# Performance work log

Hardware: AMD Instinct MI355X
Metric: run time of the kernel (lower is better)

The kernel has to match this reference:

```python
import jax, jax.numpy as jnp
import numpy as np

U, I, D, E, L = 100000, 50000, 64, 600000, 3
N = U + I  # total nodes in bipartite graph


def setup_inputs() -> dict:
    key = jax.random.key(0)
    k1, k2, k3, k4 = jax.random.split(key, 4)
    user_emb = jax.random.normal(k1, (U, D), dtype=jnp.float32) * 0.1
    item_emb = jax.random.normal(k2, (I, D), dtype=jnp.float32) * 0.1
    # random user-item interactions; symmetrize to build the (U+I)x(U+I) adjacency
    u = jax.random.randint(k3, (E,), 0, U)
    i = jax.random.randint(k4, (E,), 0, I) + U
    edge_src = jnp.concatenate([u, i])  # [2E]
    edge_dst = jnp.concatenate([i, u])  # [2E]
    # symmetric normalization: A_hat[s,d] = 1/sqrt(deg_s * deg_d)
    deg = jax.ops.segment_sum(jnp.ones((2 * E,), jnp.float32), edge_dst, num_segments=N)
    dinv = jnp.where(deg > 0, 1.0 / jnp.sqrt(deg), 0.0)
    edge_vals = dinv[edge_src] * dinv[edge_dst]
    return {
        "user_emb": user_emb,
        "item_emb": item_emb,
        "edge_src": edge_src,
        "edge_dst": edge_dst,
        "edge_vals": edge_vals,
    }


def reference(user_emb, item_emb, edge_src, edge_dst, edge_vals):
    # LightGCN propagation: ego_{k+1} = A_hat @ ego_k, then mean over the L layer outputs
    ego = jnp.concatenate([user_emb, item_emb], axis=0)  # [N, D]
    acc = jnp.zeros_like(ego)
    for _ in range(L):  # fixed small layer count
        msgs = edge_vals[:, None] * ego[edge_src]  # [2E, D] gather + scale
        ego = jax.ops.segment_sum(msgs, edge_dst, num_segments=N)  # SpMM via scatter-add
        acc = acc + ego
    mean_emb = acc / L
    return mean_emb[:U], mean_emb[U:]
```

## Files before the change

### kernel.cpp

```cpp
#include <hip/hip_runtime.h>

#define U_CNT 100000
#define I_CNT 50000
#define D_DIM 64
#define N_NODES 150000
#define CHUNK 2048
#define NBKT 586
#define SCAN_BLK 512
#define CCAP 3584

__device__ __forceinline__ float blo(unsigned u) { return __uint_as_float(u << 16); }
__device__ __forceinline__ float bhi(unsigned u) { return __uint_as_float(u & 0xFFFF0000u); }
__device__ __forceinline__ unsigned f2b(float f) {
    unsigned b = __float_as_uint(f);
    return (b + 0x7FFFu + ((b >> 16) & 1u)) >> 16;
}
__device__ __forceinline__ unsigned pack2(float a, float b) {
    return f2b(a) | (f2b(b) << 16);
}

__global__ void bucket_hist(const int* __restrict__ dst, int* __restrict__ H,
                            int NB_B, int nE,
                            const float4* __restrict__ user4,
                            const float4* __restrict__ item4,
                            uint2* __restrict__ ego0, int n4u, int n4) {
    __shared__ int h[NBKT];
    for (int i = threadIdx.x; i < NBKT; i += blockDim.x) h[i] = 0;
    __syncthreads();
    int b = blockIdx.x;
    int beg = b * CHUNK, end = min(nE, beg + CHUNK);
    for (int e = beg + (int)threadIdx.x; e < end; e += blockDim.x)
        atomicAdd(&h[dst[e] >> 8], 1);
    __syncthreads();
    for (int i = threadIdx.x; i < NBKT; i += blockDim.x) H[i * NB_B + b] = h[i];
    int gsz = gridDim.x * blockDim.x;
    for (int i = blockIdx.x * blockDim.x + threadIdx.x; i < n4; i += gsz) {
        float4 f = (i < n4u) ? user4[i] : item4[i - n4u];
        ego0[i] = make_uint2(pack2(f.x, f.y), pack2(f.z, f.w));
    }
}

__global__ void block_sums(const int* __restrict__ in, int* __restrict__ blksum, int n) {
    __shared__ int sm[SCAN_BLK];
    int i = blockIdx.x * SCAN_BLK + threadIdx.x;
    sm[threadIdx.x] = (i < n) ? in[i] : 0;
    __syncthreads();
    for (int off = SCAN_BLK / 2; off > 0; off >>= 1) {
        if (threadIdx.x < off) sm[threadIdx.x] += sm[threadIdx.x + off];
        __syncthreads();
    }
    if (threadIdx.x == 0) blksum[blockIdx.x] = sm[0];
}

__global__ void scan_blksums(const int* __restrict__ blksum, int* __restrict__ blkoff, int nb) {
    __shared__ int sm[1024];
    int t = threadIdx.x;
    int v = (t < nb) ? blksum[t] : 0;
    sm[t] = v;
    __syncthreads();
    for (int off = 1; off < 1024; off <<= 1) {
        int x = (t >= off) ? sm[t - off] : 0;
        __syncthreads();
        sm[t] += x;
        __syncthreads();
    }
    if (t < nb) blkoff[t] = sm[t] - v;
}

__global__ void scan_within(int* __restrict__ H, const int* __restrict__ blkoff, int n) {
    __shared__ int sm[SCAN_BLK];
    int i = blockIdx.x * SCAN_BLK + threadIdx.x;
    int t = threadIdx.x;
    int d = (i < n) ? H[i] : 0;
    sm[t] = d;
    __syncthreads();
    for (int off = 1; off < SCAN_BLK; off <<= 1) {
        int x = (t >= off) ? sm[t - off] : 0;
        __syncthreads();
        sm[t] += x;
        __syncthreads();
    }
    if (i < n) H[i] = blkoff[blockIdx.x] + sm[t] - d;
}

__global__ void bucket_scatter(const int* __restrict__ src, const int* __restrict__ dst,
                               const float* __restrict__ val, const int* __restrict__ Hs,
                               uint2* __restrict__ tmp, int NB_B, int nE) {
    __shared__ int cur[NBKT];
    int b = blockIdx.x;
    for (int i = threadIdx.x; i < NBKT; i += blockDim.x) cur[i] = Hs[i * NB_B + b];
    __syncthreads();
    int beg = b * CHUNK, end = min(nE, beg + CHUNK);
    for (int e = beg + (int)threadIdx.x; e < end; e += blockDim.x) {
        int d = dst[e];
        int pos = atomicAdd(&cur[d >> 8], 1);
        tmp[pos] = make_uint2((unsigned)src[e] | ((unsigned)(d & 255) << 18),
                              __float_as_uint(val[e]));
    }
}

__global__ void bucket_build(const int* __restrict__ Hs, const uint2* __restrict__ tmp,
                             int2* __restrict__ csr, int* __restrict__ row_ptr,
                             int NB_B, int nE) {
    __shared__ int hist[256];
    __shared__ int scanbuf[256];
    __shared__ int cur[256];
    __shared__ uint2 cache[CCAP];
    int bkt  = blockIdx.x;
    int base = Hs[(size_t)bkt * NB_B];
    int endp = (bkt + 1 < NBKT) ? Hs[(size_t)(bkt + 1) * NB_B] : nE;
    int size = endp - base;
    int nbins = min(256, N_NODES - bkt * 256);
    int t = threadIdx.x;

    hist[t] = 0;
    __syncthreads();
    bool cached = (size <= CCAP);
    for (int k = t; k < size; k += blockDim.x) {
        uint2 r = tmp[base + k];
        if (cached) cache[k] = r;
        atomicAdd(&hist[(r.x >> 18) & 255], 1);
    }
    __syncthreads();
    int v = hist[t];
    scanbuf[t] = v;
    __syncthreads();
    for (int off = 1; off < 256; off <<= 1) {
        int x = (t >= off) ? scanbuf[t - off] : 0;
        __syncthreads();
        scanbuf[t] += x;
        __syncthreads();
    }
    int ex = scanbuf[t] - v;
    if (t < nbins) row_ptr[bkt * 256 + t] = base + ex;
    cur[t] = ex;
    __syncthreads();
    if (bkt == NBKT - 1) {
        if (t == 0) row_ptr[N_NODES] = nE;
        if (t < 4)  csr[nE + t] = make_int2(0, 0);
    }
    for (int k = t; k < size; k += blockDim.x) {
        uint2 r = cached ? cache[k] : tmp[base + k];
        int f = (r.x >> 18) & 255;
        int p = atomicAdd(&cur[f], 1);
        csr[base + p] = make_int2((int)(r.x & 0x3FFFFu), (int)r.y);
    }
}

__global__ void deg_scatter(const int* __restrict__ row_ptr, int* __restrict__ perm) {
    __shared__ int h[256];
    __shared__ int scanbuf[256];
    int t = threadIdx.x;
    int base = blockIdx.x * 256;
    int n = base + t;
    bool valid = (n < N_NODES);
    int deg = valid ? (row_ptr[n + 1] - row_ptr[n]) : 0;
    int bin = 255 - min(deg, 255);
    h[t] = 0;
    __syncthreads();
    int rank = 0;
    if (valid) rank = atomicAdd(&h[bin], 1);
    __syncthreads();
    int v = h[t];
    scanbuf[t] = v;
    __syncthreads();
    for (int off = 1; off < 256; off <<= 1) {
        int x = (t >= off) ? scanbuf[t - off] : 0;
        __syncthreads();
        scanbuf[t] += x;
        __syncthreads();
    }
    __syncthreads();
    if (valid) {
        int ex = scanbuf[bin] - h[bin];
        perm[base + ex + rank] = n;
    }
}

__device__ __forceinline__ void fma8(float (&acc)[8], float v, uint4 g) {
    acc[0] = fmaf(v, blo(g.x), acc[0]); acc[1] = fmaf(v, bhi(g.x), acc[1]);
    acc[2] = fmaf(v, blo(g.y), acc[2]); acc[3] = fmaf(v, bhi(g.y), acc[3]);
    acc[4] = fmaf(v, blo(g.z), acc[4]); acc[5] = fmaf(v, bhi(g.z), acc[5]);
    acc[6] = fmaf(v, blo(g.w), acc[6]); acc[7] = fmaf(v, bhi(g.w), acc[7]);
}

template <int FINAL>
__global__ void lgcn_spmm(const int* __restrict__ row_ptr,
                          const int2* __restrict__ csr,
                          const uint4* __restrict__ ego_in,
                          uint4* __restrict__ ego_out,
                          const uint4* __restrict__ egoA,
                          const uint4* __restrict__ egoB,
                          float4* __restrict__ out,
                          const int* __restrict__ perm) {
    int widx = (blockIdx.x * blockDim.x + threadIdx.x) >> 3;
    int l    = threadIdx.x & 7;
    if (widx >= N_NODES) return;
    int node = perm[widx];
    int beg = row_ptr[node];
    int end = row_ptr[node + 1];

    float a0[8] = {0, 0, 0, 0, 0, 0, 0, 0};
    float a1[8] = {0, 0, 0, 0, 0, 0, 0, 0};

    int2 e0 = csr[beg], e1 = csr[beg + 1], e2 = csr[beg + 2], e3 = csr[beg + 3];
    int j = beg;
    while (j + 4 <= end) {
        uint4 x0 = ego_in[(size_t)e0.x * 8 + l];
        uint4 x1 = ego_in[(size_t)e1.x * 8 + l];
        uint4 x2 = ego_in[(size_t)e2.x * 8 + l];
        uint4 x3 = ego_in[(size_t)e3.x * 8 + l];
        int2 n0 = csr[j + 4], n1 = csr[j + 5], n2 = csr[j + 6], n3 = csr[j + 7];
        fma8(a0, __int_as_float(e0.y), x0);
        fma8(a1, __int_as_float(e1.y), x1);
        fma8(a0, __int_as_float(e2.y), x2);
        fma8(a1, __int_as_float(e3.y), x3);
        e0 = n0; e1 = n1; e2 = n2; e3 = n3;
        j += 4;
    }
    int rem = end - j;
    if (rem > 0) fma8(a0, __int_as_float(e0.y), ego_in[(size_t)e0.x * 8 + l]);
    if (rem > 1) fma8(a1, __int_as_float(e1.y), ego_in[(size_t)e1.x * 8 + l]);
    if (rem > 2) fma8(a0, __int_as_float(e2.y), ego_in[(size_t)e2.x * 8 + l]);

    float acc[8];
#pragma unroll
    for (int k = 0; k < 8; ++k) acc[k] = a0[k] + a1[k];

    if (!FINAL) {
        uint4 r;
        r.x = pack2(acc[0], acc[1]); r.y = pack2(acc[2], acc[3]);
        r.z = pack2(acc[4], acc[5]); r.w = pack2(acc[6], acc[7]);
        ego_out[(size_t)node * 8 + l] = r;
    } else {
        uint4 a = egoA[(size_t)node * 8 + l];
        uint4 b = egoB[(size_t)node * 8 + l];
        const float s = 1.0f / 3.0f;
        float4 o0, o1;
        o0.x = (blo(a.x) + blo(b.x) + acc[0]) * s;
        o0.y = (bhi(a.x) + bhi(b.x) + acc[1]) * s;
        o0.z = (blo(a.y) + blo(b.y) + acc[2]) * s;
        o0.w = (bhi(a.y) + bhi(b.y) + acc[3]) * s;
        o1.x = (blo(a.z) + blo(b.z) + acc[4]) * s;
        o1.y = (bhi(a.z) + bhi(b.z) + acc[5]) * s;
        o1.z = (blo(a.w) + blo(b.w) + acc[6]) * s;
        o1.w = (bhi(a.w) + bhi(b.w) + acc[7]) * s;
        size_t ob = (size_t)node * 16 + 2 * l;
        out[ob]     = o0;
        out[ob + 1] = o1;
    }
}

static inline size_t align_up(size_t x, size_t a) { return (x + a - 1) & ~(a - 1); }

extern "C" void kernel_launch(void* const* d_in, const int* in_sizes, int n_in,
                              void* d_out, int out_size, void* d_ws, size_t ws_size,
                              hipStream_t stream) {
    const float* user_emb  = (const float*)d_in[0];
    const float* item_emb  = (const float*)d_in[1];
    const int*   edge_src  = (const int*)d_in[2];
    const int*   edge_dst  = (const int*)d_in[3];
    const float* edge_vals = (const float*)d_in[4];
    const int    nE        = in_sizes[2];

    float* out = (float*)d_out;
    const size_t nd = (size_t)N_NODES * D_DIM;

    const int NB_B = (nE + CHUNK - 1) / CHUNK;
    const int nH   = NBKT * NB_B;
    const int NBs  = (nH + SCAN_BLK - 1) / SCAN_BLK;

    size_t off = 0;
    char* base = (char*)d_ws;
    int2*  csr     = (int2*)(base + off);  off = align_up(off + (size_t)(nE + 4) * sizeof(int2), 256);
    int*   row_ptr = (int*)(base + off);   off = align_up(off + (size_t)(N_NODES + 1) * 4, 256);
    uint2* tmp     = (uint2*)(base + off); off = align_up(off + (size_t)nE * sizeof(uint2), 256);
    int*   H       = (int*)(base + off);   off = align_up(off + (size_t)nH * 4, 256);
    int*   blksum  = (int*)(base + off);   off = align_up(off + (size_t)NBs * 4, 256);
    int*   blkoff  = (int*)(base + off);   off = align_up(off + (size_t)NBs * 4, 256);
    uint4* ego0    = (uint4*)(base + off); off = align_up(off + (size_t)N_NODES * 128, 256);
    uint4* ego_a   = (uint4*)(base + off); off = align_up(off + (size_t)N_NODES * 128, 256);
    uint4* ego_b   = (uint4*)(base + off); off = align_up(off + (size_t)N_NODES * 128, 256);
    int*   perm    = (int*)(base + off);   off = align_up(off + (size_t)N_NODES * 4, 256);

    const int block = 256;
    const int n4  = (int)(nd / 4);
    const int n4u = U_CNT * D_DIM / 4;

    bucket_hist<<<NB_B, block, 0, stream>>>(edge_dst, H, NB_B, nE,
        (const float4*)user_emb, (const float4*)item_emb, (uint2*)ego0, n4u, n4);
    block_sums<<<NBs, SCAN_BLK, 0, stream>>>(H, blksum, nH);
    scan_blksums<<<1, 1024, 0, stream>>>(blksum, blkoff, NBs);
    scan_within<<<NBs, SCAN_BLK, 0, stream>>>(H, blkoff, nH);
    bucket_scatter<<<NB_B, block, 0, stream>>>(edge_src, edge_dst, edge_vals, H, tmp, NB_B, nE);
    bucket_build<<<NBKT, block, 0, stream>>>(H, tmp, csr, row_ptr, NB_B, nE);

    deg_scatter<<<NBKT, 256, 0, stream>>>(row_ptr, perm);

    const size_t threads = (size_t)N_NODES * 8;
    const int spmm_grid = (int)((threads + block - 1) / block);

    lgcn_spmm<0><<<spmm_grid, block, 0, stream>>>(
        row_ptr, csr, ego0, ego_a, nullptr, nullptr, nullptr, perm);
    lgcn_spmm<0><<<spmm_grid, block, 0, stream>>>(
        row_ptr, csr, ego_a, ego_b, nullptr, nullptr, nullptr, perm);
    lgcn_spmm<1><<<spmm_grid, block, 0, stream>>>(
        row_ptr, csr, ego_b, nullptr, ego_a, ego_b, (float4*)out, perm);
}
```

Baseline: 265.3 us.

## Fuse degree sort into bucket_build and process four nodes per SpMM group

The per-bucket degree sort that builds perm moves into bucket_build, reusing the histogram already computed there, so the separate deg_scatter kernel launch and its re-read of row_ptr go away. The SpMM kernel now has each 8-lane group handle four consecutive nodes from perm, loading perm with an int4 load and prefetching the row pointers and first CSR entries for all four up front. This gives more memory-level parallelism per thread but launches a quarter as many groups, which lowers occupancy and can make work less balanced across groups. The code assumes N_NODES is divisible by 4.

```diff
diff --git a/kernel.cpp b/kernel.cpp
--- a/kernel.cpp
+++ b/kernel.cpp
@@ -8,6 +8,7 @@
 #define NBKT 586
 #define SCAN_BLK 512
 #define CCAP 3584
+#define NPG 4
 
 __device__ __forceinline__ float blo(unsigned u) { return __uint_as_float(u << 16); }
 __device__ __forceinline__ float bhi(unsigned u) { return __uint_as_float(u & 0xFFFF0000u); }
@@ -101,10 +102,12 @@
 
 __global__ void bucket_build(const int* __restrict__ Hs, const uint2* __restrict__ tmp,
                              int2* __restrict__ csr, int* __restrict__ row_ptr,
-                             int NB_B, int nE) {
+                             int* __restrict__ perm, int NB_B, int nE) {
     __shared__ int hist[256];
     __shared__ int scanbuf[256];
     __shared__ int cur[256];
+    __shared__ int db[256];
+    __shared__ int dbs[256];
     __shared__ uint2 cache[CCAP];
     int bkt  = blockIdx.x;
     int base = Hs[(size_t)bkt * NB_B];
@@ -114,6 +117,7 @@
     int t = threadIdx.x;
 
     hist[t] = 0;
+    db[t] = 0;
     __syncthreads();
     bool cached = (size <= CCAP);
     for (int k = t; k < size; k += blockDim.x) {
@@ -139,41 +143,30 @@
         if (t == 0) row_ptr[N_NODES] = nE;
         if (t < 4)  csr[nE + t] = make_int2(0, 0);
     }
+
+    int bin = 255 - min(v, 255);
+    int rank = 0;
+    if (t < nbins) rank = atomicAdd(&db[bin], 1);
+    __syncthreads();
+    int v2 = db[t];
+    dbs[t] = v2;
+    __syncthreads();
+    for (int off = 1; off < 256; off <<= 1) {
+        int x = (t >= off) ? dbs[t - off] : 0;
+        __syncthreads();
+        dbs[t] += x;
+        __syncthreads();
+    }
+    if (t < nbins) {
+        int ex2 = dbs[bin] - db[bin];
+        perm[bkt * 256 + ex2 + rank] = bkt * 256 + t;
+    }
+
     for (int k = t; k < size; k += blockDim.x) {
         uint2 r = cached ? cache[k] : tmp[base + k];
         int f = (r.x >> 18) & 255;
         int p = atomicAdd(&cur[f], 1);
         csr[base + p] = make_int2((int)(r.x & 0x3FFFFu), (int)r.y);
-    }
-}
-
-__global__ void deg_scatter(const int* __restrict__ row_ptr, int* __restrict__ perm) {
-    __shared__ int h[256];
-    __shared__ int scanbuf[256];
-    int t = threadIdx.x;
-    int base = blockIdx.x * 256;
-    int n = base + t;
-    bool valid = (n < N_NODES);
-    int deg = valid ? (row_ptr[n + 1] - row_ptr[n]) : 0;
-    int bin = 255 - min(deg, 255);
-    h[t] = 0;
-    __syncthreads();
-    int rank = 0;
-    if (valid) rank = atomicAdd(&h[bin], 1);
-    __syncthreads();
-    int v = h[t];
-    scanbuf[t] = v;
-    __syncthreads();
-    for (int off = 1; off < 256; off <<= 1) {
-        int x = (t >= off) ? scanbuf[t - off] : 0;
-        __syncthreads();
-        scanbuf[t] += x;
-        __syncthreads();
-    }
-    __syncthreads();
-    if (valid) {
-        int ex = scanbuf[bin] - h[bin];
-        perm[base + ex + rank] = n;
     }
 }
 
@@ -193,61 +186,80 @@
                           const uint4* __restrict__ egoB,
                           float4* __restrict__ out,
                           const int* __restrict__ perm) {
-    int widx = (blockIdx.x * blockDim.x + threadIdx.x) >> 3;
-    int l    = threadIdx.x & 7;
-    if (widx >= N_NODES) return;
-    int node = perm[widx];
-    int beg = row_ptr[node];
-    int end = row_ptr[node + 1];
-
-    float a0[8] = {0, 0, 0, 0, 0, 0, 0, 0};
-    float a1[8] = {0, 0, 0, 0, 0, 0, 0, 0};
-
-    int2 e0 = csr[beg], e1 = csr[beg + 1], e2 = csr[beg + 2], e3 = csr[beg + 3];
-    int j = beg;
-    while (j + 4 <= end) {
-        uint4 x0 = ego_in[(size_t)e0.x * 8 + l];
-        uint4 x1 = ego_in[(size_t)e1.x * 8 + l];
-        uint4 x2 = ego_in[(size_t)e2.x * 8 + l];
-        uint4 x3 = ego_in[(size_t)e3.x * 8 + l];
-        int2 n0 = csr[j + 4], n1 = csr[j + 5], n2 = csr[j + 6], n3 = csr[j + 7];
-        fma8(a0, __int_as_float(e0.y), x0);
-        fma8(a1, __int_as_float(e1.y), x1);
-        fma8(a0, __int_as_float(e2.y), x2);
-        fma8(a1, __int_as_float(e3.y), x3);
-        e0 = n0; e1 = n1; e2 = n2; e3 = n3;
-        j += 4;
-    }
-    int rem = end - j;
-    if (rem > 0) fma8(a0, __int_as_float(e0.y), ego_in[(size_t)e0.x * 8 + l]);
-    if (rem > 1) fma8(a1, __int_as_float(e1.y), ego_in[(size_t)e1.x * 8 + l]);
-    if (rem > 2) fma8(a0, __int_as_float(e2.y), ego_in[(size_t)e2.x * 8 + l]);
-
-    float acc[8];
-#pragma unroll
-    for (int k = 0; k < 8; ++k) acc[k] = a0[k] + a1[k];
-
-    if (!FINAL) {
-        uint4 r;
-        r.x = pack2(acc[0], acc[1]); r.y = pack2(acc[2], acc[3]);
-        r.z = pack2(acc[4], acc[5]); r.w = pack2(acc[6], acc[7]);
-        ego_out[(size_t)node * 8 + l] = r;
-    } else {
-        uint4 a = egoA[(size_t)node * 8 + l];
-        uint4 b = egoB[(size_t)node * 8 + l];
-        const float s = 1.0f / 3.0f;
-        float4 o0, o1;
-        o0.x = (blo(a.x) + blo(b.x) + acc[0]) * s;
-        o0.y = (bhi(a.x) + bhi(b.x) + acc[1]) * s;
-        o0.z = (blo(a.y) + blo(b.y) + acc[2]) * s;
-        o0.w = (bhi(a.y) + bhi(b.y) + acc[3]) * s;
-        o1.x = (blo(a.z) + blo(b.z) + acc[4]) * s;
-        o1.y = (bhi(a.z) + bhi(b.z) + acc[5]) * s;
-        o1.z = (blo(a.w) + blo(b.w) + acc[6]) * s;
-        o1.w = (bhi(a.w) + bhi(b.w) + acc[7]) * s;
-        size_t ob = (size_t)node * 16 + 2 * l;
-        out[ob]     = o0;
-        out[ob + 1] = o1;
+    int gid = (blockIdx.x * blockDim.x + threadIdx.x) >> 3;
+    int l   = threadIdx.x & 7;
+    int nbase = gid * NPG;
+    if (nbase >= N_NODES) return;
+
+    int4 p4 = *reinterpret_cast<const int4*>(&perm[nbase]);
+    int nodes[NPG] = {p4.x, p4.y, p4.z, p4.w};
+    int begs[NPG], ends[NPG];
+#pragma unroll
+    for (int n = 0; n < NPG; ++n) {
+        begs[n] = row_ptr[nodes[n]];
+        ends[n] = row_ptr[nodes[n] + 1];
+    }
+    int2 ce[NPG][4];
+#pragma unroll
+    for (int n = 0; n < NPG; ++n) {
+#pragma unroll
+        for (int k = 0; k < 4; ++k) ce[n][k] = csr[begs[n] + k];
+    }
+
+#pragma unroll
+    for (int n = 0; n < NPG; ++n) {
+        int node = nodes[n];
+        int beg = begs[n], end = ends[n];
+
+        float a0[8] = {0, 0, 0, 0, 0, 0, 0, 0};
+        float a1[8] = {0, 0, 0, 0, 0, 0, 0, 0};
+
+        int2 e0 = ce[n][0], e1 = ce[n][1], e2 = ce[n][2], e3 = ce[n][3];
+        int j = beg;
+        while (j + 4 <= end) {
+            uint4 x0 = ego_in[(size_t)e0.x * 8 + l];
+            uint4 x1 = ego_in[(size_t)e1.x * 8 + l];
+            uint4 x2 = ego_in[(size_t)e2.x * 8 + l];
+            uint4 x3 = ego_in[(size_t)e3.x * 8 + l];
+            int2 n0 = csr[j + 4], n1 = csr[j + 5], n2 = csr[j + 6], n3 = csr[j + 7];
+            fma8(a0, __int_as_float(e0.y), x0);
+            fma8(a1, __int_as_float(e1.y), x1);
+            fma8(a0, __int_as_float(e2.y), x2);
+            fma8(a1, __int_as_float(e3.y), x3);
+            e0 = n0; e1 = n1; e2 = n2; e3 = n3;
+            j += 4;
+        }
+        int rem = end - j;
+        if (rem > 0) fma8(a0, __int_as_float(e0.y), ego_in[(size_t)e0.x * 8 + l]);
+        if (rem > 1) fma8(a1, __int_as_float(e1.y), ego_in[(size_t)e1.x * 8 + l]);
+        if (rem > 2) fma8(a0, __int_as_float(e2.y), ego_in[(size_t)e2.x * 8 + l]);
+
+        float acc[8];
+#pragma unroll
+        for (int k = 0; k < 8; ++k) acc[k] = a0[k] + a1[k];
+
+        if (!FINAL) {
+            uint4 r;
+            r.x = pack2(acc[0], acc[1]); r.y = pack2(acc[2], acc[3]);
+            r.z = pack2(acc[4], acc[5]); r.w = pack2(acc[6], acc[7]);
+            ego_out[(size_t)node * 8 + l] = r;
+        } else {
+            uint4 a = egoA[(size_t)node * 8 + l];
+            uint4 b = egoB[(size_t)node * 8 + l];
+            const float s = 1.0f / 3.0f;
+            float4 o0, o1;
+            o0.x = (blo(a.x) + blo(b.x) + acc[0]) * s;
+            o0.y = (bhi(a.x) + bhi(b.x) + acc[1]) * s;
+            o0.z = (blo(a.y) + blo(b.y) + acc[2]) * s;
+            o0.w = (bhi(a.y) + bhi(b.y) + acc[3]) * s;
+            o1.x = (blo(a.z) + blo(b.z) + acc[4]) * s;
+            o1.y = (bhi(a.z) + bhi(b.z) + acc[5]) * s;
+            o1.z = (blo(a.w) + blo(b.w) + acc[6]) * s;
+            o1.w = (bhi(a.w) + bhi(b.w) + acc[7]) * s;
+            size_t ob = (size_t)node * 16 + 2 * l;
+            out[ob]     = o0;
+            out[ob + 1] = o1;
+        }
     }
 }
 
@@ -293,11 +305,9 @@
     scan_blksums<<<1, 1024, 0, stream>>>(blksum, blkoff, NBs);
     scan_within<<<NBs, SCAN_BLK, 0, stream>>>(H, blkoff, nH);
     bucket_scatter<<<NB_B, block, 0, stream>>>(edge_src, edge_dst, edge_vals, H, tmp, NB_B, nE);
-    bucket_build<<<NBKT, block, 0, stream>>>(H, tmp, csr, row_ptr, NB_B, nE);
-
-    deg_scatter<<<NBKT, 256, 0, stream>>>(row_ptr, perm);
-
-    const size_t threads = (size_t)N_NODES * 8;
+    bucket_build<<<NBKT, block, 0, stream>>>(H, tmp, csr, row_ptr, perm, NB_B, nE);
+
+    const size_t threads = ((size_t)N_NODES / NPG) * 8;
     const int spmm_grid = (int)((threads + block - 1) / block);
 
     lgcn_spmm<0><<<spmm_grid, block, 0, stream>>>(
```

Result: no change. 269.0 us (+1.4%).
